# Optimization experiments

Hardware: AMD Instinct MI355X
Metric: run time of the kernel (lower is better)

The kernel has to match this reference:

```python
import jax, jax.numpy as jnp
import numpy as np

B, T, D, H = 32, 1024, 128, 4
DH = D // H  # per-head dim = 32
NEG = -(2.0**32) + 1.0  # padding value used by SoftmaxWeightedSum
LN_EPS = 1e-9


def setup_inputs() -> dict:
    key = jax.random.key(0)
    k1, k2, k3, k4 = jax.random.split(key, 4)
    x = jax.random.normal(k1, (B, T, D), dtype=jnp.float32)
    keys_length = jax.random.randint(k2, (B, 1), 1, T + 1, dtype=jnp.int32)
    W = jax.random.normal(k3, (D, 3 * D), dtype=jnp.float32) * 0.05
    W_output = jax.random.normal(k4, (D, D), dtype=jnp.float32) * 0.05
    gamma = jnp.ones((D,), dtype=jnp.float32)
    beta = jnp.zeros((D,), dtype=jnp.float32)
    return {"x": x, "keys_length": keys_length, "W": W,
            "W_output": W_output, "gamma": gamma, "beta": beta}


def reference(x, keys_length, W, W_output, gamma, beta):
    # QKV projection: [B,T,D] @ [D,3D] -> [B,T,3D]
    qkv = jnp.einsum('btd,de->bte', x, W)
    q, k, v = jnp.split(qkv, 3, axis=-1)

    # tf.split(axis=2)+concat(axis=0) == head-major [H,B,T,DH]
    def to_heads(t):
        return t.reshape(B, T, H, DH).transpose(2, 0, 1, 3)
    q, k, v = to_heads(q), to_heads(k), to_heads(v)

    # DotAttention with scale by sqrt(per-head key dim)
    scores = jnp.einsum('hbqd,hbkd->hbqk', q, k) / jnp.sqrt(jnp.float32(DH))

    # key padding mask from sequence lengths: [B,T] bool
    key_mask = jnp.arange(T)[None, :] < keys_length  # keys_length is [B,1]
    # causal (future_binding) lower-triangular mask: [T,T]
    causal = jnp.tril(jnp.ones((T, T), dtype=bool))
    mask = causal[None, None, :, :] & key_mask[None, :, None, :]  # [1,B,T,T] -> broadcast over H
    scores = jnp.where(mask, scores, NEG)

    attn = jax.nn.softmax(scores, axis=-1)  # [H,B,T,T]
    out = jnp.einsum('hbqk,hbkd->hbqd', attn, v)  # [H,B,T,DH]

    # concat heads back to channel dim: [B,T,D]
    out = out.transpose(1, 2, 0, 3).reshape(B, T, D)
    out = jnp.einsum('btd,de->bte', out, W_output)

    # residual + layernorm (dropout is identity at inference)
    out = out + x
    mean = jnp.mean(out, axis=-1, keepdims=True)
    var = jnp.var(out, axis=-1, keepdims=True)
    out = (out - mean) * jax.lax.rsqrt(var + LN_EPS) * gamma + beta
    return out
```

## Files before the change

kernel.cpp:

```cpp
#include <hip/hip_runtime.h>
#include <hip/hip_bf16.h>

#define B_ 32
#define T_ 1024
#define D_ 128
#define H_ 4
#define DH_ 32

typedef unsigned short ushort_t;
typedef unsigned int uint_t;
typedef unsigned short ushort4_t __attribute__((ext_vector_type(4)));
typedef unsigned short ushort8_t __attribute__((ext_vector_type(8)));
typedef short short8_t __attribute__((ext_vector_type(8)));
typedef float float4_t __attribute__((ext_vector_type(4)));
typedef unsigned int uint4_t __attribute__((ext_vector_type(4)));

__device__ __forceinline__ ushort_t f2bf_bits(float f) {
    __hip_bfloat16 h = __float2bfloat16(f);
    return *reinterpret_cast<ushort_t*>(&h);
}
__device__ __forceinline__ uint_t pk_bf16(float hi, float lo) {
    return __builtin_amdgcn_perm(__float_as_uint(hi), __float_as_uint(lo),
                                 0x07060302u);
}
#if __has_builtin(__builtin_amdgcn_exp2f)
__device__ __forceinline__ float fast_exp2(float x) { return __builtin_amdgcn_exp2f(x); }
#else
__device__ __forceinline__ float fast_exp2(float x) { return exp2f(x); }
#endif

__global__ __launch_bounds__(256) void qkv_mfma(
    const float* __restrict__ x, const float* __restrict__ W,
    const float* __restrict__ Wo,
    __hip_bfloat16* __restrict__ qws, __hip_bfloat16* __restrict__ kws,
    __hip_bfloat16* __restrict__ vtws, ushort_t* __restrict__ Wot)
{
    __shared__ ushort_t xst[64][136];
    __shared__ ushort_t qkA[2][16 * 200];
    __shared__ ushort_t qkB[2][16 * 72];

    if (blockIdx.x >= 512) {
        const int t = (blockIdx.x - 512) * 256 + threadIdx.x;
        const int nt = t >> 8, kc = (t >> 6) & 3, lane = t & 63;
        const int tq = lane >> 4, ti = lane & 15;
        const int n = nt * 16 + ti;
        const float* wo = Wo + (size_t)(kc * 32 + tq * 8) * 128 + n;
        ushort4_t a, b2;
        a[0]  = f2bf_bits(wo[0 * 128]); a[1]  = f2bf_bits(wo[1 * 128]);
        a[2]  = f2bf_bits(wo[2 * 128]); a[3]  = f2bf_bits(wo[3 * 128]);
        b2[0] = f2bf_bits(wo[4 * 128]); b2[1] = f2bf_bits(wo[5 * 128]);
        b2[2] = f2bf_bits(wo[6 * 128]); b2[3] = f2bf_bits(wo[7 * 128]);
        *(ushort4_t*)(Wot + (size_t)t * 8)     = a;
        *(ushort4_t*)(Wot + (size_t)t * 8 + 4) = b2;
        return;
    }

    const int tid = threadIdx.x;
    const int lane = tid & 63;
    const int i15 = lane & 15, quad = lane >> 4;
    const int wid = tid >> 6;
    const int wpart = wid & 1;
    const int pairIdx = wid >> 1;
    const int gw = blockIdx.x * 4 + wid;
    const int row0 = (gw >> 1) * 32;

    {
        const float* xblk = x + (size_t)blockIdx.x * 64 * 128;
        #pragma unroll
        for (int it = 0; it < 8; ++it) {
            const int idx = (it * 256 + tid) * 4;
            const int row = idx >> 7, col = idx & 127;
            const float4 v = *(const float4*)(xblk + idx);
            ushort4_t s;
            s[0] = f2bf_bits(v.x); s[1] = f2bf_bits(v.y);
            s[2] = f2bf_bits(v.z); s[3] = f2bf_bits(v.w);
            *(ushort4_t*)(&xst[row][col]) = s;
        }
    }
    __syncthreads();

    short8_t af[2][4];
    #pragma unroll
    for (int rg = 0; rg < 2; ++rg)
        #pragma unroll
        for (int kc = 0; kc < 4; ++kc)
            af[rg][kc] = *(const short8_t*)(&xst[pairIdx * 32 + rg * 16 + i15][kc * 32 + quad * 8]);

    float4_t acc[2][12];
    #pragma unroll
    for (int rg = 0; rg < 2; ++rg)
        #pragma unroll
        for (int nt = 0; nt < 12; ++nt) acc[rg][nt] = (float4_t){0.f, 0.f, 0.f, 0.f};

    #pragma unroll
    for (int nt = 0; nt < 12; ++nt) {
        const int n = wpart * 192 + nt * 16 + i15;
        const float* wcol = W + n;
        #pragma unroll
        for (int kc = 0; kc < 4; ++kc) {
            const float* wk = wcol + (size_t)(kc * 32 + quad * 8) * 384;
            const float w0 = wk[0 * 384], w1 = wk[1 * 384];
            const float w2 = wk[2 * 384], w3 = wk[3 * 384];
            const float w4 = wk[4 * 384], w5 = wk[5 * 384];
            const float w6 = wk[6 * 384], w7 = wk[7 * 384];
            uint4_t up;
            up[0] = pk_bf16(w1, w0); up[1] = pk_bf16(w3, w2);
            up[2] = pk_bf16(w5, w4); up[3] = pk_bf16(w7, w6);
            const short8_t bf = *reinterpret_cast<const short8_t*>(&up);
            acc[0][nt] = __builtin_amdgcn_mfma_f32_16x16x32_bf16(af[0][kc], bf, acc[0][nt], 0, 0, 0);
            acc[1][nt] = __builtin_amdgcn_mfma_f32_16x16x32_bf16(af[1][kc], bf, acc[1][nt], 0, 0, 0);
        }
    }

    const float scale = 0.17677669529663687f * 1.4426950408889634f;
    const int t = lane >> 2, c4 = lane & 3;

    #pragma unroll
    for (int rg = 0; rg < 2; ++rg) {
        const int r0 = row0 + rg * 16;
        const int b = r0 >> 10, t0 = r0 & 1023;
        if (wpart == 0) {
            ushort_t* Ls = qkA[pairIdx];
            #pragma unroll
            for (int nt = 0; nt < 12; ++nt) {
                const int col = nt * 16 + i15;
                const float sc = (nt < 8) ? scale : 1.f;
                #pragma unroll
                for (int r = 0; r < 4; ++r)
                    Ls[(quad * 4 + r) * 200 + col] = f2bf_bits(acc[rg][nt][r] * sc);
            }
            #pragma unroll
            for (int it = 0; it < 6; ++it) {
                const int col8 = it * 4 + c4;
                const ushort8_t v8 = *(const ushort8_t*)(Ls + t * 200 + col8 * 8);
                __hip_bfloat16* base = (it < 4) ? qws : kws;
                const int h = (it < 4) ? it : (it - 4);
                *(ushort8_t*)((ushort_t*)base +
                    ((size_t)(b * H_ + h) * T_ + t0 + t) * DH_ + c4 * 8) = v8;
            }
        } else {
            ushort_t* Ls = qkB[pairIdx];
            #pragma unroll
            for (int nt = 0; nt < 12; ++nt) {
                if (nt < 4) {
                    const int col = nt * 16 + i15;
                    #pragma unroll
                    for (int r = 0; r < 4; ++r)
                        Ls[(quad * 4 + r) * 72 + col] = f2bf_bits(acc[rg][nt][r]);
                } else {
                    const int ch = nt * 16 + i15 - 64;
                    const int h = ch >> 5, dh = ch & 31;
                    ushort4_t pk;
                    #pragma unroll
                    for (int r = 0; r < 4; ++r) pk[r] = f2bf_bits(acc[rg][nt][r]);
                    const int k_ = t0 + quad * 4;
                    const int c_ = k_ >> 6;
                    const int g_ = ((k_ & 63) >> 5) | ((dh >> 4) << 1);
                    const int lp = (dh & 15) | (((k_ & 31) >> 3) << 4);
                    *(ushort4_t*)((ushort_t*)vtws +
                        (((size_t)(b * H_ + h) * 16 + c_) * 4 + g_) * 512 +
                        lp * 8 + (k_ & 7)) = pk;
                }
            }
            #pragma unroll
            for (int it = 0; it < 2; ++it) {
                const int col8 = it * 4 + c4;
                const ushort8_t v8 = *(const ushort8_t*)(Ls + t * 72 + col8 * 8);
                *(ushort8_t*)((ushort_t*)kws +
                    ((size_t)(b * H_ + 2 + it) * T_ + t0 + t) * DH_ + c4 * 8) = v8;
            }
        }
    }
}

__global__ __launch_bounds__(256, 2) void attn_proj_ln(
    const ushort_t* __restrict__ qws, const ushort_t* __restrict__ kws,
    const ushort_t* __restrict__ vtws, const int* __restrict__ keys_length,
    const ushort_t* __restrict__ Wot, const float* __restrict__ x,
    const float* __restrict__ gamma, const float* __restrict__ beta,
    float* __restrict__ out)
{
    __shared__ ushort_t plds[4][32 * 72];
    __shared__ ushort_t att[32 * 128];

    const int wid = threadIdx.x >> 6;
    const int lane = threadIdx.x & 63;
    const int i15 = lane & 15, quad = lane >> 4;
    const int b = blockIdx.x & 31;
    const int st = 31 - (blockIdx.x >> 5);
    const int qbase = st * 32;
    const int h = wid;
    const int bh = b * 4 + h;
    const int len = keys_length[b];

    const ushort_t* Qb = qws + (size_t)bh * T_ * DH_;
    const ushort_t* Kb = kws + (size_t)bh * T_ * DH_;
    const ushort_t* Vtb = vtws + (size_t)bh * 32768;

    const short8_t qfA = *(const short8_t*)(Qb + (size_t)(qbase + i15) * DH_ + quad * 8);
    const short8_t qfB = *(const short8_t*)(Qb + (size_t)(qbase + 16 + i15) * DH_ + quad * 8);

    const int kend    = min(qbase + 32, len);
    const int nch     = (kend + 63) >> 6;
    const int limAmax = min(qbase + 16, len);
    const int nfullA  = min(qbase + 1, len) >> 6;
    const int nfullB  = min(qbase + 17, len) >> 6;
    const int limA    = min(qbase + i15 + 1, len);
    const int limB    = min(qbase + 16 + i15 + 1, len);

    ushort_t* pl = plds[h];

    float4_t oA0 = {0,0,0,0}, oA1 = {0,0,0,0}, oB0 = {0,0,0,0}, oB1 = {0,0,0,0};
    float laccA = 0.f, laccB = 0.f;
    const float4_t zero = {0,0,0,0};

    short8_t kf[4], vf[4];
    {
        #pragma unroll
        for (int g = 0; g < 4; ++g)
            kf[g] = *(const short8_t*)(Kb + (size_t)(g * 16 + i15) * DH_ + quad * 8);
        #pragma unroll
        for (int g = 0; g < 4; ++g)
            vf[g] = *(const short8_t*)(Vtb + g * 512 + lane * 8);
    }

    for (int c = 0; c < nch; ++c) {
        const int k0 = c * 64;
        const bool doA = (k0 < limAmax);

        float4_t sB[4], sA[4];
        #pragma unroll
        for (int g = 0; g < 4; ++g)
            sB[g] = __builtin_amdgcn_mfma_f32_16x16x32_bf16(kf[g], qfB, zero, 0, 0, 0);
        if (doA) {
            #pragma unroll
            for (int g = 0; g < 4; ++g)
                sA[g] = __builtin_amdgcn_mfma_f32_16x16x32_bf16(kf[g], qfA, zero, 0, 0, 0);
        }

        short8_t kf2[4], vf2[4];
        const int c2 = c + 1;
        if (c2 < nch) {
            const int k2 = c2 * 64;
            #pragma unroll
            for (int g = 0; g < 4; ++g)
                kf2[g] = *(const short8_t*)(Kb + (size_t)(k2 + g * 16 + i15) * DH_ + quad * 8);
            #pragma unroll
            for (int g = 0; g < 4; ++g)
                vf2[g] = *(const short8_t*)(Vtb + (size_t)c2 * 2048 + g * 512 + lane * 8);
        }
        __builtin_amdgcn_sched_barrier(0);

        {
            const bool fullB = (c < nfullB);
            ushort_t* prow = pl + (16 + i15) * 72 + quad * 4;
            #pragma unroll
            for (int g = 0; g < 4; ++g) {
                float p0 = fast_exp2(sB[g][0]), p1 = fast_exp2(sB[g][1]);
                float p2 = fast_exp2(sB[g][2]), p3 = fast_exp2(sB[g][3]);
                if (!fullB) {
                    const int d = limB - (k0 + g * 16 + quad * 4);
                    p0 = (d > 0) ? p0 : 0.f; p1 = (d > 1) ? p1 : 0.f;
                    p2 = (d > 2) ? p2 : 0.f; p3 = (d > 3) ? p3 : 0.f;
                }
                laccB += (p0 + p1) + (p2 + p3);
                uint2 w; w.x = pk_bf16(p1, p0); w.y = pk_bf16(p3, p2);
                *(uint2*)(prow + g * 16) = w;
            }
        }
        if (doA) {
            const bool fullA = (c < nfullA);
            ushort_t* prow = pl + i15 * 72 + quad * 4;
            #pragma unroll
            for (int g = 0; g < 4; ++g) {
                float p0 = fast_exp2(sA[g][0]), p1 = fast_exp2(sA[g][1]);
                float p2 = fast_exp2(sA[g][2]), p3 = fast_exp2(sA[g][3]);
                if (!fullA) {
                    const int d = limA - (k0 + g * 16 + quad * 4);
                    p0 = (d > 0) ? p0 : 0.f; p1 = (d > 1) ? p1 : 0.f;
                    p2 = (d > 2) ? p2 : 0.f; p3 = (d > 3) ? p3 : 0.f;
                }
                laccA += (p0 + p1) + (p2 + p3);
                uint2 w; w.x = pk_bf16(p1, p0); w.y = pk_bf16(p3, p2);
                *(uint2*)(prow + g * 16) = w;
            }
        }

        {
            const short8_t pfB0 = *(const short8_t*)(pl + (16 + i15) * 72 + quad * 8);
            const short8_t pfB1 = *(const short8_t*)(pl + (16 + i15) * 72 + 32 + quad * 8);
            oB0 = __builtin_amdgcn_mfma_f32_16x16x32_bf16(pfB0, vf[0], oB0, 0, 0, 0);
            oB0 = __builtin_amdgcn_mfma_f32_16x16x32_bf16(pfB1, vf[1], oB0, 0, 0, 0);
            oB1 = __builtin_amdgcn_mfma_f32_16x16x32_bf16(pfB0, vf[2], oB1, 0, 0, 0);
            oB1 = __builtin_amdgcn_mfma_f32_16x16x32_bf16(pfB1, vf[3], oB1, 0, 0, 0);
        }
        if (doA) {
            const short8_t pfA0 = *(const short8_t*)(pl + i15 * 72 + quad * 8);
            const short8_t pfA1 = *(const short8_t*)(pl + i15 * 72 + 32 + quad * 8);
            oA0 = __builtin_amdgcn_mfma_f32_16x16x32_bf16(pfA0, vf[0], oA0, 0, 0, 0);
            oA0 = __builtin_amdgcn_mfma_f32_16x16x32_bf16(pfA1, vf[1], oA0, 0, 0, 0);
            oA1 = __builtin_amdgcn_mfma_f32_16x16x32_bf16(pfA0, vf[2], oA1, 0, 0, 0);
            oA1 = __builtin_amdgcn_mfma_f32_16x16x32_bf16(pfA1, vf[3], oA1, 0, 0, 0);
        }

        if (c2 < nch) {
            #pragma unroll
            for (int g = 0; g < 4; ++g) { kf[g] = kf2[g]; vf[g] = vf2[g]; }
        }
    }

    laccA += __shfl_xor(laccA, 16, 64); laccA += __shfl_xor(laccA, 32, 64);
    laccB += __shfl_xor(laccB, 16, 64); laccB += __shfl_xor(laccB, 32, 64);

    #pragma unroll
    for (int r = 0; r < 4; ++r) {
        const int q = quad * 4 + r;
        const float invA = 1.f / __shfl(laccA, q, 64);
        const float invB = 1.f / __shfl(laccB, q, 64);
        const int colL = h * 32 + i15, colH = h * 32 + 16 + i15;
        char* ab = (char*)att;
        *(ushort_t*)(ab + ((q * 256 + colL * 2) ^ ((q & 7) << 4)))        = f2bf_bits(oA0[r] * invA);
        *(ushort_t*)(ab + ((q * 256 + colH * 2) ^ ((q & 7) << 4)))        = f2bf_bits(oA1[r] * invA);
        *(ushort_t*)(ab + (((16 + q) * 256 + colL * 2) ^ ((q & 7) << 4))) = f2bf_bits(oB0[r] * invB);
        *(ushort_t*)(ab + (((16 + q) * 256 + colH * 2) ^ ((q & 7) << 4))) = f2bf_bits(oB1[r] * invB);
    }
    __syncthreads();

    if (wid < 2) {
        const int lr = wid * 16 + i15;
        short8_t af[4];
        #pragma unroll
        for (int kc = 0; kc < 4; ++kc)
            af[kc] = *(const short8_t*)((const char*)att +
                ((lr * 256 + kc * 64 + quad * 16) ^ ((lr & 7) << 4)));

        float4_t acc[8];
        #pragma unroll
        for (int nt = 0; nt < 8; ++nt) acc[nt] = (float4_t){0.f, 0.f, 0.f, 0.f};

        #pragma unroll
        for (int nt = 0; nt < 8; ++nt) {
            #pragma unroll
            for (int kc = 0; kc < 4; ++kc) {
                const short8_t bf = *(const short8_t*)(Wot +
                    (size_t)((nt * 4 + kc) * 64 + lane) * 8);
                acc[nt] = __builtin_amdgcn_mfma_f32_16x16x32_bf16(af[kc], bf, acc[nt], 0, 0, 0);
            }
        }

        float g[8], be[8];
        #pragma unroll
        for (int nt = 0; nt < 8; ++nt) {
            g[nt] = gamma[nt * 16 + i15];
            be[nt] = beta[nt * 16 + i15];
        }

        const int m0 = b * T_ + qbase + wid * 16;
        #pragma unroll
        for (int r = 0; r < 4; ++r) {
            const int m = m0 + quad * 4 + r;
            float y[8];
            float s1 = 0.f, s2 = 0.f;
            #pragma unroll
            for (int nt = 0; nt < 8; ++nt) {
                y[nt] = acc[nt][r] + x[(size_t)m * 128 + nt * 16 + i15];
                s1 += y[nt];
                s2 += y[nt] * y[nt];
            }
            #pragma unroll
            for (int off = 1; off < 16; off <<= 1) {
                s1 += __shfl_xor(s1, off, 64);
                s2 += __shfl_xor(s2, off, 64);
            }
            const float mean = s1 * (1.f / 128.f);
            const float var = s2 * (1.f / 128.f) - mean * mean;
            const float rstd = rsqrtf(var + 1e-9f);
            #pragma unroll
            for (int nt = 0; nt < 8; ++nt)
                out[(size_t)m * 128 + nt * 16 + i15] = (y[nt] - mean) * rstd * g[nt] + be[nt];
        }
    }
}

extern "C" void kernel_launch(void* const* d_in, const int* in_sizes, int n_in,
                              void* d_out, int out_size, void* d_ws, size_t ws_size,
                              hipStream_t stream) {
    const float* x      = (const float*)d_in[0];
    const int* keys_len = (const int*)d_in[1];
    const float* W      = (const float*)d_in[2];
    const float* Wo     = (const float*)d_in[3];
    const float* gamma  = (const float*)d_in[4];
    const float* beta   = (const float*)d_in[5];
    float* out          = (float*)d_out;

    const size_t seg = (size_t)B_ * H_ * T_ * DH_;
    __hip_bfloat16* qws  = (__hip_bfloat16*)d_ws;
    __hip_bfloat16* kws  = qws + seg;
    __hip_bfloat16* vtws = qws + 2 * seg;
    ushort_t* Wot = (ushort_t*)(qws + 3 * seg);

    qkv_mfma<<<520, 256, 0, stream>>>(x, W, Wo, qws, kws, vtws, Wot);
    attn_proj_ln<<<B_ * (T_ / 32), 256, 0, stream>>>(
        (const ushort_t*)qws, (const ushort_t*)kws, (const ushort_t*)vtws,
        keys_len, Wot, x, gamma, beta, out);
}
```

Before: 114.3 us.

## Halve attention query tile to 16 rows and split output projection across waves

Each attention block now handles 16 query rows instead of 32, doubling the grid to 2048 blocks. Each wave (one head) processes a single 16-row MFMA tile, and the A/B dual-tile logic is removed. The output projection and LayerNorm epilogue is split by column half across two waves, with row partial sums exchanged through shared memory and an extra barrier. The aim is more parallelism and better load balance under the causal mask, and lower shared memory per block. The cost is that K/V chunks are reloaded by twice as many blocks, with less reuse per load.

```diff
diff --git a/kernel.cpp b/kernel.cpp
--- a/kernel.cpp
+++ b/kernel.cpp
@@ -180,15 +180,15 @@
     const float* __restrict__ gamma, const float* __restrict__ beta,
     float* __restrict__ out)
 {
-    __shared__ ushort_t plds[4][32 * 72];
-    __shared__ ushort_t att[32 * 128];
+    __shared__ ushort_t plds[4][16 * 72];
+    __shared__ ushort_t att[16 * 128];
 
     const int wid = threadIdx.x >> 6;
     const int lane = threadIdx.x & 63;
     const int i15 = lane & 15, quad = lane >> 4;
     const int b = blockIdx.x & 31;
-    const int st = 31 - (blockIdx.x >> 5);
-    const int qbase = st * 32;
+    const int st = 63 - (blockIdx.x >> 5);
+    const int qbase = st * 16;
     const int h = wid;
     const int bh = b * 4 + h;
     const int len = keys_length[b];
@@ -198,20 +198,16 @@
     const ushort_t* Vtb = vtws + (size_t)bh * 32768;
 
     const short8_t qfA = *(const short8_t*)(Qb + (size_t)(qbase + i15) * DH_ + quad * 8);
-    const short8_t qfB = *(const short8_t*)(Qb + (size_t)(qbase + 16 + i15) * DH_ + quad * 8);
-
-    const int kend    = min(qbase + 32, len);
-    const int nch     = (kend + 63) >> 6;
-    const int limAmax = min(qbase + 16, len);
-    const int nfullA  = min(qbase + 1, len) >> 6;
-    const int nfullB  = min(qbase + 17, len) >> 6;
-    const int limA    = min(qbase + i15 + 1, len);
-    const int limB    = min(qbase + 16 + i15 + 1, len);
+
+    const int kend   = min(qbase + 16, len);
+    const int nch    = (kend + 63) >> 6;
+    const int nfullA = min(qbase + 1, len) >> 6;
+    const int limA   = min(qbase + i15 + 1, len);
 
     ushort_t* pl = plds[h];
 
-    float4_t oA0 = {0,0,0,0}, oA1 = {0,0,0,0}, oB0 = {0,0,0,0}, oB1 = {0,0,0,0};
-    float laccA = 0.f, laccB = 0.f;
+    float4_t oA0 = {0,0,0,0}, oA1 = {0,0,0,0};
+    float laccA = 0.f;
     const float4_t zero = {0,0,0,0};
 
     short8_t kf[4], vf[4];
@@ -226,17 +222,11 @@
 
     for (int c = 0; c < nch; ++c) {
         const int k0 = c * 64;
-        const bool doA = (k0 < limAmax);
-
-        float4_t sB[4], sA[4];
+
+        float4_t sA[4];
         #pragma unroll
         for (int g = 0; g < 4; ++g)
-            sB[g] = __builtin_amdgcn_mfma_f32_16x16x32_bf16(kf[g], qfB, zero, 0, 0, 0);
-        if (doA) {
-            #pragma unroll
-            for (int g = 0; g < 4; ++g)
-                sA[g] = __builtin_amdgcn_mfma_f32_16x16x32_bf16(kf[g], qfA, zero, 0, 0, 0);
-        }
+            sA[g] = __builtin_amdgcn_mfma_f32_16x16x32_bf16(kf[g], qfA, zero, 0, 0, 0);
 
         short8_t kf2[4], vf2[4];
         const int c2 = c + 1;
@@ -252,23 +242,6 @@
         __builtin_amdgcn_sched_barrier(0);
 
         {
-            const bool fullB = (c < nfullB);
-            ushort_t* prow = pl + (16 + i15) * 72 + quad * 4;
-            #pragma unroll
-            for (int g = 0; g < 4; ++g) {
-                float p0 = fast_exp2(sB[g][0]), p1 = fast_exp2(sB[g][1]);
-                float p2 = fast_exp2(sB[g][2]), p3 = fast_exp2(sB[g][3]);
-                if (!fullB) {
-                    const int d = limB - (k0 + g * 16 + quad * 4);
-                    p0 = (d > 0) ? p0 : 0.f; p1 = (d > 1) ? p1 : 0.f;
-                    p2 = (d > 2) ? p2 : 0.f; p3 = (d > 3) ? p3 : 0.f;
-                }
-                laccB += (p0 + p1) + (p2 + p3);
-                uint2 w; w.x = pk_bf16(p1, p0); w.y = pk_bf16(p3, p2);
-                *(uint2*)(prow + g * 16) = w;
-            }
-        }
-        if (doA) {
             const bool fullA = (c < nfullA);
             ushort_t* prow = pl + i15 * 72 + quad * 4;
             #pragma unroll
@@ -287,14 +260,6 @@
         }
 
         {
-            const short8_t pfB0 = *(const short8_t*)(pl + (16 + i15) * 72 + quad * 8);
-            const short8_t pfB1 = *(const short8_t*)(pl + (16 + i15) * 72 + 32 + quad * 8);
-            oB0 = __builtin_amdgcn_mfma_f32_16x16x32_bf16(pfB0, vf[0], oB0, 0, 0, 0);
-            oB0 = __builtin_amdgcn_mfma_f32_16x16x32_bf16(pfB1, vf[1], oB0, 0, 0, 0);
-            oB1 = __builtin_amdgcn_mfma_f32_16x16x32_bf16(pfB0, vf[2], oB1, 0, 0, 0);
-            oB1 = __builtin_amdgcn_mfma_f32_16x16x32_bf16(pfB1, vf[3], oB1, 0, 0, 0);
-        }
-        if (doA) {
             const short8_t pfA0 = *(const short8_t*)(pl + i15 * 72 + quad * 8);
             const short8_t pfA1 = *(const short8_t*)(pl + i15 * 72 + 32 + quad * 8);
             oA0 = __builtin_amdgcn_mfma_f32_16x16x32_bf16(pfA0, vf[0], oA0, 0, 0, 0);
@@ -310,74 +275,84 @@
     }
 
     laccA += __shfl_xor(laccA, 16, 64); laccA += __shfl_xor(laccA, 32, 64);
-    laccB += __shfl_xor(laccB, 16, 64); laccB += __shfl_xor(laccB, 32, 64);
 
     #pragma unroll
     for (int r = 0; r < 4; ++r) {
         const int q = quad * 4 + r;
         const float invA = 1.f / __shfl(laccA, q, 64);
-        const float invB = 1.f / __shfl(laccB, q, 64);
         const int colL = h * 32 + i15, colH = h * 32 + 16 + i15;
         char* ab = (char*)att;
-        *(ushort_t*)(ab + ((q * 256 + colL * 2) ^ ((q & 7) << 4)))        = f2bf_bits(oA0[r] * invA);
-        *(ushort_t*)(ab + ((q * 256 + colH * 2) ^ ((q & 7) << 4)))        = f2bf_bits(oA1[r] * invA);
-        *(ushort_t*)(ab + (((16 + q) * 256 + colL * 2) ^ ((q & 7) << 4))) = f2bf_bits(oB0[r] * invB);
-        *(ushort_t*)(ab + (((16 + q) * 256 + colH * 2) ^ ((q & 7) << 4))) = f2bf_bits(oB1[r] * invB);
+        *(ushort_t*)(ab + ((q * 256 + colL * 2) ^ ((q & 7) << 4))) = f2bf_bits(oA0[r] * invA);
+        *(ushort_t*)(ab + ((q * 256 + colH * 2) ^ ((q & 7) << 4))) = f2bf_bits(oA1[r] * invA);
     }
     __syncthreads();
 
+    float2* pbuf = (float2*)(&plds[0][0]);
+    const int ch = wid;
+    float y[4][4], s1r[4], s2r[4], g[4], be[4];
     if (wid < 2) {
-        const int lr = wid * 16 + i15;
         short8_t af[4];
         #pragma unroll
         for (int kc = 0; kc < 4; ++kc)
             af[kc] = *(const short8_t*)((const char*)att +
-                ((lr * 256 + kc * 64 + quad * 16) ^ ((lr & 7) << 4)));
-
-        float4_t acc[8];
-        #pragma unroll
-        for (int nt = 0; nt < 8; ++nt) acc[nt] = (float4_t){0.f, 0.f, 0.f, 0.f};
-
-        #pragma unroll
-        for (int nt = 0; nt < 8; ++nt) {
+                ((i15 * 256 + kc * 64 + quad * 16) ^ ((i15 & 7) << 4)));
+
+        float4_t acc[4];
+        #pragma unroll
+        for (int nt = 0; nt < 4; ++nt) acc[nt] = (float4_t){0.f, 0.f, 0.f, 0.f};
+
+        #pragma unroll
+        for (int nt = 0; nt < 4; ++nt) {
+            const int ntg = ch * 4 + nt;
             #pragma unroll
             for (int kc = 0; kc < 4; ++kc) {
                 const short8_t bf = *(const short8_t*)(Wot +
-                    (size_t)((nt * 4 + kc) * 64 + lane) * 8);
+                    (size_t)((ntg * 4 + kc) * 64 + lane) * 8);
                 acc[nt] = __builtin_amdgcn_mfma_f32_16x16x32_bf16(af[kc], bf, acc[nt], 0, 0, 0);
             }
         }
 
-        float g[8], be[8];
-        #pragma unroll
-        for (int nt = 0; nt < 8; ++nt) {
-            g[nt] = gamma[nt * 16 + i15];
-            be[nt] = beta[nt * 16 + i15];
-        }
-
-        const int m0 = b * T_ + qbase + wid * 16;
+        #pragma unroll
+        for (int nt = 0; nt < 4; ++nt) {
+            g[nt]  = gamma[ch * 64 + nt * 16 + i15];
+            be[nt] = beta[ch * 64 + nt * 16 + i15];
+        }
+
+        const int m0 = b * T_ + qbase;
         #pragma unroll
         for (int r = 0; r < 4; ++r) {
             const int m = m0 + quad * 4 + r;
-            float y[8];
             float s1 = 0.f, s2 = 0.f;
             #pragma unroll
-            for (int nt = 0; nt < 8; ++nt) {
-                y[nt] = acc[nt][r] + x[(size_t)m * 128 + nt * 16 + i15];
-                s1 += y[nt];
-                s2 += y[nt] * y[nt];
+            for (int nt = 0; nt < 4; ++nt) {
+                y[r][nt] = acc[nt][r] + x[(size_t)m * 128 + ch * 64 + nt * 16 + i15];
+                s1 += y[r][nt];
+                s2 += y[r][nt] * y[r][nt];
             }
             #pragma unroll
             for (int off = 1; off < 16; off <<= 1) {
                 s1 += __shfl_xor(s1, off, 64);
                 s2 += __shfl_xor(s2, off, 64);
             }
+            s1r[r] = s1; s2r[r] = s2;
+            if (i15 == 0) pbuf[ch * 16 + quad * 4 + r] = (float2){s1, s2};
+        }
+    }
+    __syncthreads();
+    if (wid < 2) {
+        const int m0 = b * T_ + qbase;
+        #pragma unroll
+        for (int r = 0; r < 4; ++r) {
+            const int m = m0 + quad * 4 + r;
+            const float2 o = pbuf[(1 - ch) * 16 + quad * 4 + r];
+            const float s1 = s1r[r] + o.x, s2 = s2r[r] + o.y;
             const float mean = s1 * (1.f / 128.f);
             const float var = s2 * (1.f / 128.f) - mean * mean;
             const float rstd = rsqrtf(var + 1e-9f);
             #pragma unroll
-            for (int nt = 0; nt < 8; ++nt)
-                out[(size_t)m * 128 + nt * 16 + i15] = (y[nt] - mean) * rstd * g[nt] + be[nt];
+            for (int nt = 0; nt < 4; ++nt)
+                out[(size_t)m * 128 + ch * 64 + nt * 16 + i15] =
+                    (y[r][nt] - mean) * rstd * g[nt] + be[nt];
         }
     }
 }
@@ -400,7 +375,7 @@
     ushort_t* Wot = (ushort_t*)(qws + 3 * seg);
 
     qkv_mfma<<<520, 256, 0, stream>>>(x, W, Wo, qws, kws, vtws, Wot);
-    attn_proj_ln<<<B_ * (T_ / 32), 256, 0, stream>>>(
+    attn_proj_ln<<<B_ * (T_ / 16), 256, 0, stream>>>(
         (const ushort_t*)qws, (const ushort_t*)kws, (const ushort_t*)vtws,
         keys_len, Wot, x, gamma, beta, out);
 }
```

Measured after the change: 122.5 us. 1.07x slower.
